# Optimization experiments

Hardware: AMD Instinct MI355X
Metric: run time of the kernel (lower is better)

Reference implementation:

```python
import jax, jax.numpy as jnp
import numpy as np


def setup_inputs() -> dict:
    key = jax.random.key(0)
    ks = jax.random.split(key, 5)
    B, T, C, HS = 8, 2048, 1024, 64
    return {
        "x_q": jax.random.normal(ks[0], (B, T, C), dtype=jnp.float32),
        "x_kv": jax.random.normal(ks[1], (B, T, C), dtype=jnp.float32),
        "Wq": jax.random.normal(ks[2], (C, HS), dtype=jnp.float32) * (C ** -0.5),
        "Wk": jax.random.normal(ks[3], (C, HS), dtype=jnp.float32) * (C ** -0.5),
        "Wv": jax.random.normal(ks[4], (C, HS), dtype=jnp.float32) * (C ** -0.5),
    }


def reference(x_q, x_kv, Wq, Wk, Wv):
    # x_q, x_kv: [B, T, C]; W*: [C, HS]
    B, T, C = x_q.shape
    q = jnp.einsum("btc,ch->bth", x_q, Wq)   # [B, T, HS]
    k = jnp.einsum("btc,ch->bth", x_kv, Wk)  # [B, T, HS]
    v = jnp.einsum("btc,ch->bth", x_kv, Wv)  # [B, T, HS]
    # NOTE: original scales by d_model**-0.5 (C), not head_size**-0.5
    wei = jnp.einsum("bqh,bkh->bqk", q, k) * (C ** -0.5)  # [B, T, T]
    causal = jnp.tril(jnp.ones((T, T), dtype=bool))
    wei = jnp.where(causal, wei, -jnp.inf)
    wei = jax.nn.softmax(wei, axis=-1)
    out = jnp.einsum("bqk,bkh->bqh", wei, v)  # [B, T, HS]
    return out
```

## Files before the change

kernel.cpp:

```cpp
#include <hip/hip_runtime.h>

typedef __bf16 bf16_t;
typedef __bf16 bf16x8 __attribute__((ext_vector_type(8)));
typedef float f32x4 __attribute__((ext_vector_type(4)));
typedef unsigned short u16x4 __attribute__((ext_vector_type(4)));

#define B_ 8
#define T_ 2048
#define C_ 1024
#define HS_ 64

#define MFMA __builtin_amdgcn_mfma_f32_16x16x32_bf16

__device__ __forceinline__ float fast_exp2(float x) {
#if __has_builtin(__builtin_amdgcn_exp2f)
  return __builtin_amdgcn_exp2f(x);
#else
  return exp2f(x);
#endif
}

__global__ __launch_bounds__(256) void repack_w(
    const float* __restrict__ Wq, const float* __restrict__ Wk,
    const float* __restrict__ Wv, bf16_t* __restrict__ pq,
    bf16_t* __restrict__ pk, bf16_t* __restrict__ pv) {
  const float* W = (blockIdx.y == 0) ? Wq : ((blockIdx.y == 1) ? Wk : Wv);
  bf16_t* P = (blockIdx.y == 0) ? pq : ((blockIdx.y == 1) ? pk : pv);
  int t = blockIdx.x * 256 + threadIdx.x;
  int lane = t & 63, nt = (t >> 6) & 3, kc = t >> 8;
  int quad = lane >> 4, ln = lane & 15;
  bf16x8 v;
#pragma unroll
  for (int j = 0; j < 8; ++j)
    v[j] = (bf16_t)W[(kc * 32 + quad * 8 + j) * HS_ + nt * 16 + ln];
  *(bf16x8*)(P + (size_t)t * 8) = v;
}

__global__ __launch_bounds__(256) void proj_mfma(
    const float* __restrict__ xq, const float* __restrict__ xkv,
    const bf16_t* __restrict__ pq, const bf16_t* __restrict__ pk,
    const bf16_t* __restrict__ pv, bf16_t* __restrict__ q,
    bf16_t* __restrict__ k, bf16_t* __restrict__ vT) {
  const int rt = blockIdx.x;
  const bool is_kv = (blockIdx.y != 0);
  const int w = threadIdx.x >> 6, lane = threadIdx.x & 63;
  const int quad = lane >> 4, ln = lane & 15;
  const int m0 = rt * 64 + w * 16;
  const float* x = is_kv ? xkv : xq;
  const bf16_t* p0 = is_kv ? pk : pq;

  f32x4 acc0[4], acc1[4];
#pragma unroll
  for (int nt = 0; nt < 4; ++nt) {
    acc0[nt] = (f32x4){0.f, 0.f, 0.f, 0.f};
    acc1[nt] = (f32x4){0.f, 0.f, 0.f, 0.f};
  }

  for (int kc = 0; kc < 32; ++kc) {
    const float* xf = x + (size_t)(m0 + ln) * C_ + kc * 32 + quad * 8;
    f32x4 lo = *(const f32x4*)xf;
    f32x4 hi = *(const f32x4*)(xf + 4);
    bf16x8 a;
#pragma unroll
    for (int j = 0; j < 4; ++j) {
      a[j] = (bf16_t)lo[j];
      a[4 + j] = (bf16_t)hi[j];
    }
#pragma unroll
    for (int nt = 0; nt < 4; ++nt) {
      bf16x8 b = *(const bf16x8*)(p0 + ((size_t)(kc * 4 + nt) * 64 + lane) * 8);
      acc0[nt] = MFMA(a, b, acc0[nt], 0, 0, 0);
    }
    if (is_kv) {
#pragma unroll
      for (int nt = 0; nt < 4; ++nt) {
        bf16x8 b = *(const bf16x8*)(pv + ((size_t)(kc * 4 + nt) * 64 + lane) * 8);
        acc1[nt] = MFMA(a, b, acc1[nt], 0, 0, 0);
      }
    }
  }

  if (!is_kv) {
#pragma unroll
    for (int nt = 0; nt < 4; ++nt)
#pragma unroll
      for (int r = 0; r < 4; ++r)
        q[(size_t)(m0 + quad * 4 + r) * HS_ + nt * 16 + ln] = (bf16_t)acc0[nt][r];
  } else {
#pragma unroll
    for (int nt = 0; nt < 4; ++nt)
#pragma unroll
      for (int r = 0; r < 4; ++r)
        k[(size_t)(m0 + quad * 4 + r) * HS_ + nt * 16 + ln] = (bf16_t)acc0[nt][r];
    const int bb = m0 >> 11, t0 = m0 & (T_ - 1);
#pragma unroll
    for (int nt = 0; nt < 4; ++nt) {
      u16x4 pk4;
#pragma unroll
      for (int r = 0; r < 4; ++r) {
        bf16_t h = (bf16_t)acc1[nt][r];
        pk4[r] = *(unsigned short*)&h;
      }
      *(u16x4*)((unsigned short*)vT + ((size_t)(bb * HS_ + nt * 16 + ln)) * T_ +
                t0 + quad * 4) = pk4;
    }
  }
}

__global__ __launch_bounds__(256) void attn_mfma(
    const bf16_t* __restrict__ q, const bf16_t* __restrict__ k,
    const bf16_t* __restrict__ vT, float* __restrict__ out) {
  __shared__ bf16_t p_lds[4][16][80];
  __shared__ float o_buf[3][16][64];
  __shared__ float l_buf[4][16][16];

  const int b = blockIdx.x >> 7;
  const int gq = blockIdx.x & 127;
  const int w = threadIdx.x >> 6, lane = threadIdx.x & 63;
  const int quad = lane >> 4, ln = lane & 15;
  const int qr0 = gq * 16;
  const size_t bt = (size_t)b * T_;
  const int td = gq >> 2;

  bf16x8 aq[2];
#pragma unroll
  for (int hc = 0; hc < 2; ++hc)
    aq[hc] = *(const bf16x8*)(q + (bt + qr0 + ln) * HS_ + hc * 32 + quad * 8);

  f32x4 o_acc[4];
  float l_part[4] = {0.f, 0.f, 0.f, 0.f};
#pragma unroll
  for (int nt = 0; nt < 4; ++nt) o_acc[nt] = (f32x4){0.f, 0.f, 0.f, 0.f};
  const float scl = 0.03125f * 1.44269504088896340736f;

  for (int t = w; t <= td; t += 4) {
    const int kr0 = t * 64;

    f32x4 s[4];
#pragma unroll
    for (int nt = 0; nt < 4; ++nt) s[nt] = (f32x4){0.f, 0.f, 0.f, 0.f};
#pragma unroll
    for (int hc = 0; hc < 2; ++hc)
#pragma unroll
      for (int nt = 0; nt < 4; ++nt) {
        bf16x8 bk = *(const bf16x8*)(k + (bt + kr0 + nt * 16 + ln) * HS_ +
                                     hc * 32 + quad * 8);
        s[nt] = MFMA(aq[hc], bk, s[nt], 0, 0, 0);
      }

    const bool diag = (t == td);
#pragma unroll
    for (int nt = 0; nt < 4; ++nt)
#pragma unroll
      for (int r = 0; r < 4; ++r) {
        float e = fast_exp2(s[nt][r] * scl);
        if (diag && (kr0 + nt * 16 + ln > qr0 + quad * 4 + r)) e = 0.f;
        l_part[r] += e;
        p_lds[w][quad * 4 + r][nt * 16 + ln] = (bf16_t)e;
      }

#pragma unroll
    for (int kc = 0; kc < 2; ++kc) {
      bf16x8 ap = *(const bf16x8*)&p_lds[w][ln][kc * 32 + quad * 8];
#pragma unroll
      for (int nt = 0; nt < 4; ++nt) {
        bf16x8 bv = *(const bf16x8*)(vT + ((size_t)(b * HS_ + nt * 16 + ln)) * T_ +
                                     kr0 + kc * 32 + quad * 8);
        o_acc[nt] = MFMA(ap, bv, o_acc[nt], 0, 0, 0);
      }
    }
  }

  if (w != 0) {
#pragma unroll
    for (int nt = 0; nt < 4; ++nt)
#pragma unroll
      for (int r = 0; r < 4; ++r)
        o_buf[w - 1][quad * 4 + r][nt * 16 + ln] = o_acc[nt][r];
  }
#pragma unroll
  for (int r = 0; r < 4; ++r) l_buf[w][quad * 4 + r][ln] = l_part[r];
  __syncthreads();

  if (w == 0) {
#pragma unroll
    for (int ww = 0; ww < 3; ++ww)
#pragma unroll
      for (int nt = 0; nt < 4; ++nt)
#pragma unroll
        for (int r = 0; r < 4; ++r)
          o_acc[nt][r] += o_buf[ww][quad * 4 + r][nt * 16 + ln];
    float l_row[4];
#pragma unroll
    for (int r = 0; r < 4; ++r) {
      float v = l_buf[0][quad * 4 + r][ln] + l_buf[1][quad * 4 + r][ln] +
                l_buf[2][quad * 4 + r][ln] + l_buf[3][quad * 4 + r][ln];
#pragma unroll
      for (int off = 1; off < 16; off <<= 1) v += __shfl_xor(v, off);
      l_row[r] = v;
    }
#pragma unroll
    for (int nt = 0; nt < 4; ++nt)
#pragma unroll
      for (int r = 0; r < 4; ++r)
        out[(bt + qr0 + quad * 4 + r) * HS_ + nt * 16 + ln] =
            o_acc[nt][r] / l_row[r];
  }
}

extern "C" void kernel_launch(void* const* d_in, const int* in_sizes, int n_in,
                              void* d_out, int out_size, void* d_ws,
                              size_t ws_size, hipStream_t stream) {
  (void)in_sizes; (void)n_in; (void)out_size; (void)ws_size;
  const float* xq = (const float*)d_in[0];
  const float* xkv = (const float*)d_in[1];
  const float* Wq = (const float*)d_in[2];
  const float* Wk = (const float*)d_in[3];
  const float* Wv = (const float*)d_in[4];
  float* out = (float*)d_out;

  char* ws = (char*)d_ws;
  bf16_t* q = (bf16_t*)ws;
  bf16_t* kk = (bf16_t*)(ws + (2u << 20));
  bf16_t* vT = (bf16_t*)(ws + (4u << 20));
  bf16_t* pq = (bf16_t*)(ws + (6u << 20));
  bf16_t* pk = (bf16_t*)(ws + (6u << 20) + (128u << 10));
  bf16_t* pv = (bf16_t*)(ws + (6u << 20) + (256u << 10));

  repack_w<<<dim3(32, 3), 256, 0, stream>>>(Wq, Wk, Wv, pq, pk, pv);
  proj_mfma<<<dim3(256, 2), 256, 0, stream>>>(xq, xkv, pq, pk, pv, q, kk, vT);
  attn_mfma<<<dim3(1024), 256, 0, stream>>>(q, kk, vT, out);
}
```

Baseline: 240.0 us.

## Double waves per block with split-K in projection and wider key split in attention

The projection kernel now runs 8 waves per block. The two halves of the waves each handle half of the C reduction, and their partial accumulators are combined through shared memory. The attention kernel also moves to 8 waves, each striding over key tiles by 8, with wider LDS buffers for the cross-wave reduction of outputs and row sums. The aim is more in-flight memory traffic and better load balance across the causal key range, at the cost of extra LDS reduction work and a block barrier.

```diff
diff --git a/kernel.cpp b/kernel.cpp
--- a/kernel.cpp
+++ b/kernel.cpp
@@ -36,16 +36,20 @@
   *(bf16x8*)(P + (size_t)t * 8) = v;
 }
 
-__global__ __launch_bounds__(256) void proj_mfma(
+__global__ __launch_bounds__(512) void proj_mfma(
     const float* __restrict__ xq, const float* __restrict__ xkv,
     const bf16_t* __restrict__ pq, const bf16_t* __restrict__ pk,
     const bf16_t* __restrict__ pv, bf16_t* __restrict__ q,
     bf16_t* __restrict__ k, bf16_t* __restrict__ vT) {
+  __shared__ float r0[4][16][68];
+  __shared__ float r1[4][16][68];
+
   const int rt = blockIdx.x;
   const bool is_kv = (blockIdx.y != 0);
-  const int w = threadIdx.x >> 6, lane = threadIdx.x & 63;
+  const int wv = threadIdx.x >> 6, lane = threadIdx.x & 63;
+  const int wr = wv & 3, kh = wv >> 2;
   const int quad = lane >> 4, ln = lane & 15;
-  const int m0 = rt * 64 + w * 16;
+  const int m0 = rt * 64 + wr * 16;
   const float* x = is_kv ? xkv : xq;
   const bf16_t* p0 = is_kv ? pk : pq;
 
@@ -56,7 +60,7 @@
     acc1[nt] = (f32x4){0.f, 0.f, 0.f, 0.f};
   }
 
-  for (int kc = 0; kc < 32; ++kc) {
+  for (int kc = kh * 16; kc < kh * 16 + 16; ++kc) {
     const float* xf = x + (size_t)(m0 + ln) * C_ + kc * 32 + quad * 8;
     f32x4 lo = *(const f32x4*)xf;
     f32x4 hi = *(const f32x4*)(xf + 4);
@@ -80,6 +84,26 @@
     }
   }
 
+  if (kh == 1) {
+#pragma unroll
+    for (int nt = 0; nt < 4; ++nt)
+#pragma unroll
+      for (int r = 0; r < 4; ++r) {
+        r0[wr][quad * 4 + r][nt * 16 + ln] = acc0[nt][r];
+        if (is_kv) r1[wr][quad * 4 + r][nt * 16 + ln] = acc1[nt][r];
+      }
+  }
+  __syncthreads();
+  if (kh != 0) return;
+
+#pragma unroll
+  for (int nt = 0; nt < 4; ++nt)
+#pragma unroll
+    for (int r = 0; r < 4; ++r) {
+      acc0[nt][r] += r0[wr][quad * 4 + r][nt * 16 + ln];
+      if (is_kv) acc1[nt][r] += r1[wr][quad * 4 + r][nt * 16 + ln];
+    }
+
   if (!is_kv) {
 #pragma unroll
     for (int nt = 0; nt < 4; ++nt)
@@ -107,12 +131,12 @@
   }
 }
 
-__global__ __launch_bounds__(256) void attn_mfma(
+__global__ __launch_bounds__(512) void attn_mfma(
     const bf16_t* __restrict__ q, const bf16_t* __restrict__ k,
     const bf16_t* __restrict__ vT, float* __restrict__ out) {
-  __shared__ bf16_t p_lds[4][16][80];
-  __shared__ float o_buf[3][16][64];
-  __shared__ float l_buf[4][16][16];
+  __shared__ bf16_t p_lds[8][16][80];
+  __shared__ float o_buf[7][16][68];
+  __shared__ float l_buf[8][16][16];
 
   const int b = blockIdx.x >> 7;
   const int gq = blockIdx.x & 127;
@@ -133,7 +157,7 @@
   for (int nt = 0; nt < 4; ++nt) o_acc[nt] = (f32x4){0.f, 0.f, 0.f, 0.f};
   const float scl = 0.03125f * 1.44269504088896340736f;
 
-  for (int t = w; t <= td; t += 4) {
+  for (int t = w; t <= td; t += 8) {
     const int kr0 = t * 64;
 
     f32x4 s[4];
@@ -184,7 +208,7 @@
 
   if (w == 0) {
 #pragma unroll
-    for (int ww = 0; ww < 3; ++ww)
+    for (int ww = 0; ww < 7; ++ww)
 #pragma unroll
       for (int nt = 0; nt < 4; ++nt)
 #pragma unroll
@@ -193,8 +217,9 @@
     float l_row[4];
 #pragma unroll
     for (int r = 0; r < 4; ++r) {
-      float v = l_buf[0][quad * 4 + r][ln] + l_buf[1][quad * 4 + r][ln] +
-                l_buf[2][quad * 4 + r][ln] + l_buf[3][quad * 4 + r][ln];
+      float v = 0.f;
+#pragma unroll
+      for (int ww = 0; ww < 8; ++ww) v += l_buf[ww][quad * 4 + r][ln];
 #pragma unroll
       for (int off = 1; off < 16; off <<= 1) v += __shfl_xor(v, off);
       l_row[r] = v;
@@ -228,6 +253,6 @@
   bf16_t* pv = (bf16_t*)(ws + (6u << 20) + (256u << 10));
 
   repack_w<<<dim3(32, 3), 256, 0, stream>>>(Wq, Wk, Wv, pq, pk, pv);
-  proj_mfma<<<dim3(256, 2), 256, 0, stream>>>(xq, xkv, pq, pk, pv, q, kk, vT);
-  attn_mfma<<<dim3(1024), 256, 0, stream>>>(q, kk, vT, out);
-}
+  proj_mfma<<<dim3(256, 2), 512, 0, stream>>>(xq, xkv, pq, pk, pv, q, kk, vT);
+  attn_mfma<<<dim3(1024), 512, 0, stream>>>(q, kk, vT, out);
+}
```

After: 221.4 us. 1.08x faster.
